# Kernel tuning notes

Measured on AMD Instinct MI355X. Metric: run time of the kernel, lower is better.

The kernel has to match this reference:

```python
import jax, jax.numpy as jnp
import numpy as np

N = 50000      # nodes
E = 800000     # directed edges (avg degree 16)
M = 10000      # hyperedges
P = 200000     # hypergraph incidence pairs (~4 per vertex)
D_IN = 64
D_OUT = 64
NEG_SLOPE = 0.2


def setup_inputs() -> dict:
    key = jax.random.key(0)
    ks = jax.random.split(key, 9)
    X = jax.random.normal(ks[0], (N, D_IN), jnp.float32)
    theta_w = jax.random.normal(ks[1], (D_OUT, D_IN), jnp.float32) / np.float32(np.sqrt(D_IN))
    theta_b = jax.random.normal(ks[2], (D_OUT,), jnp.float32) * 0.01
    a_src = jax.random.normal(ks[3], (D_OUT,), jnp.float32) / np.float32(np.sqrt(D_OUT))
    a_dst = jax.random.normal(ks[4], (D_OUT,), jnp.float32) / np.float32(np.sqrt(D_OUT))
    e_src = jax.random.randint(ks[5], (E,), 0, N, jnp.int32)
    e_dst = jax.random.randint(ks[6], (E,), 0, N, jnp.int32)
    inc_v = jax.random.randint(ks[7], (P,), 0, N, jnp.int32)
    inc_e = jax.random.randint(ks[8], (P,), 0, M, jnp.int32)
    return {"X": X, "theta_w": theta_w, "theta_b": theta_b, "a_src": a_src,
            "a_dst": a_dst, "e_src": e_src, "e_dst": e_dst,
            "inc_v": inc_v, "inc_e": inc_e}


def reference(X, theta_w, theta_b, a_src, a_dst, e_src, e_dst, inc_v, inc_e):
    # theta: Linear(in, out)
    Xp = X @ theta_w.T + theta_b                      # [N, D_OUT]
    # atten_src/atten_dst: Linear(out, 1, bias=False) -> per-node scalars
    s_src = Xp @ a_src                                # [N]
    s_dst = Xp @ a_dst                                # [N]
    # edge attention scores: gather + leaky_relu (dropout = identity in eval)
    score = jax.nn.leaky_relu(s_src[e_src] + s_dst[e_dst], NEG_SLOPE)  # [E]
    # segment softmax over incoming edges of each destination node
    seg_max = jax.ops.segment_max(score, e_dst, num_segments=N)
    seg_max = jax.lax.stop_gradient(jnp.where(jnp.isfinite(seg_max), seg_max, 0.0))
    w = jnp.exp(score - seg_max[e_dst])               # [E]
    denom = jax.ops.segment_sum(w, e_dst, num_segments=N)
    w = w / denom[e_dst]
    # weighted scatter-sum of source features (g.v2v softmax_then_sum)
    X_g = jax.ops.segment_sum(w[:, None] * Xp[e_src], e_dst, num_segments=N)
    # HGNN smoothing: D_v^{-1/2} H D_e^{-1} H^T D_v^{-1/2} Xp  (unit hyperedge weights)
    ones_p = jnp.ones((P,), Xp.dtype)
    dv = jax.ops.segment_sum(ones_p, inc_v, num_segments=N)
    de = jax.ops.segment_sum(ones_p, inc_e, num_segments=M)
    dv_isqrt = jnp.where(dv > 0, jax.lax.rsqrt(jnp.maximum(dv, 1.0)), 0.0)
    de_inv = jnp.where(de > 0, 1.0 / jnp.maximum(de, 1.0), 0.0)
    Xs = Xp * dv_isqrt[:, None]                        # [N, D_OUT]
    He = jax.ops.segment_sum(Xs[inc_v], inc_e, num_segments=M) * de_inv[:, None]  # [M, D_OUT]
    X_hg = jax.ops.segment_sum(He[inc_e], inc_v, num_segments=N) * dv_isqrt[:, None]
    X1 = (X_g + X_hg) * 0.5
    return jax.nn.elu(X1)
```

## Files before the change

### kernel.cpp

```cpp
#include <hip/hip_runtime.h>
#include <math.h>

#define DD 64

typedef __attribute__((ext_vector_type(8))) short bf16x8;
typedef __attribute__((ext_vector_type(4))) float f32x4;

__device__ __forceinline__ unsigned short f2bf(float x) {
    unsigned int u = __float_as_uint(x);
    u += 0x7fffu + ((u >> 16) & 1u);
    return (unsigned short)(u >> 16);
}
__device__ __forceinline__ float bflo(unsigned int u) { return __uint_as_float(u << 16); }
__device__ __forceinline__ float bfhi(unsigned int u) { return __uint_as_float(u & 0xffff0000u); }

__global__ __launch_bounds__(256) void k_gemm(
    const float* __restrict__ X, const float* __restrict__ W,
    const float* __restrict__ bias, const float* __restrict__ a_src,
    const float* __restrict__ a_dst, unsigned short* __restrict__ Xp_bf,
    float* __restrict__ s_src, float* __restrict__ s_dst, int N)
{
    int t = threadIdx.x;
    int lane = t & 63;
    int col = lane & 15;
    int kq  = lane >> 4;
    int rowbase = kq * 4;

    bf16x8 bfrag[4][2];
    float bj[4], asr[4], adr[4];
    #pragma unroll
    for (int jt = 0; jt < 4; ++jt) {
        int j = jt * 16 + col;
        #pragma unroll
        for (int ks = 0; ks < 2; ++ks) {
            const float* wp = W + j * DD + ks * 32 + kq * 8;
            float4 w0 = *(const float4*)wp;
            float4 w1 = *(const float4*)(wp + 4);
            bf16x8 bb;
            bb[0] = (short)f2bf(w0.x); bb[1] = (short)f2bf(w0.y);
            bb[2] = (short)f2bf(w0.z); bb[3] = (short)f2bf(w0.w);
            bb[4] = (short)f2bf(w1.x); bb[5] = (short)f2bf(w1.y);
            bb[6] = (short)f2bf(w1.z); bb[7] = (short)f2bf(w1.w);
            bfrag[jt][ks] = bb;
        }
        bj[jt]  = bias[j];
        asr[jt] = a_src[j];
        adr[jt] = a_dst[j];
    }

    int wave  = (blockIdx.x * 256 + t) >> 6;
    int nwave = (gridDim.x * 256) >> 6;
    int ntiles = (N + 15) >> 4;
    for (int tile = wave; tile < ntiles; tile += nwave) {
        int r0 = tile * 16;
        int rl = r0 + col;
        if (rl >= N) rl = N - 1;
        const float* xp = X + (size_t)rl * DD + kq * 8;
        float4 x0 = *(const float4*)xp;
        float4 x1 = *(const float4*)(xp + 4);
        float4 x2 = *(const float4*)(xp + 32);
        float4 x3 = *(const float4*)(xp + 36);
        bf16x8 a0, a1;
        a0[0] = (short)f2bf(x0.x); a0[1] = (short)f2bf(x0.y);
        a0[2] = (short)f2bf(x0.z); a0[3] = (short)f2bf(x0.w);
        a0[4] = (short)f2bf(x1.x); a0[5] = (short)f2bf(x1.y);
        a0[6] = (short)f2bf(x1.z); a0[7] = (short)f2bf(x1.w);
        a1[0] = (short)f2bf(x2.x); a1[1] = (short)f2bf(x2.y);
        a1[2] = (short)f2bf(x2.z); a1[3] = (short)f2bf(x2.w);
        a1[4] = (short)f2bf(x3.x); a1[5] = (short)f2bf(x3.y);
        a1[6] = (short)f2bf(x3.z); a1[7] = (short)f2bf(x3.w);

        f32x4 acc[4];
        #pragma unroll
        for (int jt = 0; jt < 4; ++jt) {
            f32x4 c = {bj[jt], bj[jt], bj[jt], bj[jt]};
            c = __builtin_amdgcn_mfma_f32_16x16x32_bf16(a0, bfrag[jt][0], c, 0, 0, 0);
            c = __builtin_amdgcn_mfma_f32_16x16x32_bf16(a1, bfrag[jt][1], c, 0, 0, 0);
            acc[jt] = c;
        }

        int orow = r0 + rowbase;
        #pragma unroll
        for (int jt = 0; jt < 4; ++jt) {
            #pragma unroll
            for (int r = 0; r < 4; ++r) {
                int rr = orow + r;
                if (rr < N)
                    Xp_bf[(size_t)rr * DD + jt * 16 + col] = f2bf(acc[jt][r]);
            }
        }

        float vs[4], vd[4];
        #pragma unroll
        for (int r = 0; r < 4; ++r) {
            vs[r] = acc[0][r] * asr[0] + acc[1][r] * asr[1]
                  + acc[2][r] * asr[2] + acc[3][r] * asr[3];
            vd[r] = acc[0][r] * adr[0] + acc[1][r] * adr[1]
                  + acc[2][r] * adr[2] + acc[3][r] * adr[3];
        }
        #pragma unroll
        for (int off = 1; off < 16; off <<= 1) {
            #pragma unroll
            for (int r = 0; r < 4; ++r) {
                vs[r] += __shfl_xor(vs[r], off, 64);
                vd[r] += __shfl_xor(vd[r], off, 64);
            }
        }
        if (col == 0) {
            #pragma unroll
            for (int r = 0; r < 4; ++r) {
                int rr = orow + r;
                if (rr < N) { s_src[rr] = vs[r]; s_dst[rr] = vd[r]; }
            }
        }
    }
}

__global__ __launch_bounds__(256) void k_count(
    const int* __restrict__ e_dst, const int* __restrict__ inc_e,
    const int* __restrict__ inc_v, int* __restrict__ hist_g,
    int* __restrict__ hist_ie, int* __restrict__ hist_iv,
    int E, int P, int N, int M)
{
    __shared__ int cnt[128];
    int b = blockIdx.x;
    const int* key; int n, B, SH, nblk, blk; int* hist;
    if (b < 256)      { key = e_dst; n = E; B = (N + 511) >> 9; SH = 9; nblk = 256; blk = b;       hist = hist_g;  }
    else if (b < 384) { key = inc_e; n = P; B = (M + 255) >> 8; SH = 8; nblk = 128; blk = b - 256; hist = hist_ie; }
    else              { key = inc_v; n = P; B = (N + 511) >> 9; SH = 9; nblk = 128; blk = b - 384; hist = hist_iv; }
    for (int i = threadIdx.x; i < B; i += 256) cnt[i] = 0;
    __syncthreads();
    int chunk = (n + nblk - 1) / nblk;
    int s = blk * chunk, e = min(n, s + chunk);
    for (int i = s + threadIdx.x; i < e; i += 256)
        atomicAdd(&cnt[key[i] >> SH], 1);
    __syncthreads();
    for (int i = threadIdx.x; i < B; i += 256)
        hist[i * nblk + blk] = cnt[i];
}

__device__ void block_scan4(int* a, int len)
{
    __shared__ int wtot[16];
    __shared__ int carry_s;
    int tid = threadIdx.x, lane = tid & 63, wid = tid >> 6;
    if (tid == 0) carry_s = 0;
    __syncthreads();
    for (int base = 0; base < len; base += 4096) {
        int i0 = base + tid * 4;
        int v[4];
        #pragma unroll
        for (int k = 0; k < 4; ++k) { int i = i0 + k; v[k] = (i < len) ? a[i] : 0; }
        int s = v[0] + v[1] + v[2] + v[3];
        int incl = s;
        #pragma unroll
        for (int off = 1; off < 64; off <<= 1) {
            int t = __shfl_up(incl, off, 64);
            if (lane >= off) incl += t;
        }
        if (lane == 63) wtot[wid] = incl;
        __syncthreads();
        int carry = carry_s;
        int woff = 0;
        for (int wj = 0; wj < wid; ++wj) woff += wtot[wj];
        int excl = carry + woff + incl - s;
        int run = excl;
        #pragma unroll
        for (int k = 0; k < 4; ++k) { int i = i0 + k; if (i < len) a[i] = run; run += v[k]; }
        __syncthreads();
        if (tid == 1023) carry_s = run;
        __syncthreads();
    }
    if (tid == 0) a[len] = carry_s;
}

__global__ __launch_bounds__(1024) void k_scan3(
    int* h0, int l0, int* h1, int l1, int* h2, int l2)
{
    if (blockIdx.x == 0)      block_scan4(h0, l0);
    else if (blockIdx.x == 1) block_scan4(h1, l1);
    else                      block_scan4(h2, l2);
}

__global__ __launch_bounds__(256) void k_scat(
    const int* __restrict__ e_dst, const int* __restrict__ e_src,
    const int* __restrict__ inc_e, const int* __restrict__ inc_v,
    const int* __restrict__ hist_g, const int* __restrict__ hist_ie,
    const int* __restrict__ hist_iv,
    int2* __restrict__ pg, int2* __restrict__ pie, int2* __restrict__ piv,
    int E, int P, int N, int M)
{
    __shared__ int cur[128];
    int b = blockIdx.x;
    const int *key, *pay, *base; int2* out;
    int n, B, SH, nblk, blk;
    if (b < 256)      { key = e_dst; pay = e_src; n = E; B = (N + 511) >> 9; SH = 9; nblk = 256; blk = b;       base = hist_g;  out = pg;  }
    else if (b < 384) { key = inc_e; pay = inc_v; n = P; B = (M + 255) >> 8; SH = 8; nblk = 128; blk = b - 256; base = hist_ie; out = pie; }
    else              { key = inc_v; pay = inc_e; n = P; B = (N + 511) >> 9; SH = 9; nblk = 128; blk = b - 384; base = hist_iv; out = piv; }
    for (int i = threadIdx.x; i < B; i += 256) cur[i] = base[i * nblk + blk];
    __syncthreads();
    int chunk = (n + nblk - 1) / nblk;
    int s = blk * chunk, e = min(n, s + chunk);
    for (int i = s + threadIdx.x; i < e; i += 256) {
        int k = key[i];
        int pos = atomicAdd(&cur[k >> SH], 1);
        out[pos] = make_int2(k, pay[i]);
    }
}

__global__ __launch_bounds__(256) void k_fine(
    const int* __restrict__ hist_g, const int* __restrict__ hist_ie,
    const int* __restrict__ hist_iv,
    const int2* __restrict__ pg, const int2* __restrict__ pie,
    const int2* __restrict__ piv,
    int* __restrict__ src_sorted, int* __restrict__ v_sorted,
    int* __restrict__ e_sorted,
    int* __restrict__ start_g, int* __restrict__ start_e,
    int* __restrict__ start_v,
    float* __restrict__ dein, float* __restrict__ dvis, int N, int M)
{
    __shared__ int lh[513];
    __shared__ int lc[512];
    __shared__ int lwt[4];
    __shared__ int lout[10240];
    int Bg = (N + 511) >> 9, Bie = (M + 255) >> 8;
    int b = blockIdx.x, tid = threadIdx.x;
    const int* base; const int2* pr; int* outp; int* startp; float* inv;
    int K, nblk, b0, NK, mode;
    if (b < Bg)            { base = hist_g;  pr = pg;  outp = src_sorted; startp = start_g; inv = nullptr; K = 512; nblk = 256; b0 = b;            NK = N; mode = 0; }
    else if (b < Bg + Bie) { base = hist_ie; pr = pie; outp = v_sorted;   startp = start_e; inv = dein;    K = 256; nblk = 128; b0 = b - Bg;       NK = M; mode = 2; }
    else                   { base = hist_iv; pr = piv; outp = e_sorted;   startp = start_v; inv = dvis;    K = 512; nblk = 128; b0 = b - Bg - Bie; NK = N; mode = 1; }

    int pbase = base[b0 * nblk], pend = base[(b0 + 1) * nblk];
    int cnt = pend - pbase;
    for (int i = tid; i < K; i += 256) { lh[i] = 0; lc[i] = 0; }
    __syncthreads();
    for (int i = tid; i < cnt; i += 256)
        atomicAdd(&lh[pr[pbase + i].x & (K - 1)], 1);
    __syncthreads();

    int per = K >> 8;
    int i0 = tid * per;
    int a0 = lh[i0], a1 = (per == 2) ? lh[i0 + 1] : 0;
    int ssum = a0 + a1;
    int lane = tid & 63, wid = tid >> 6;
    int incl = ssum;
    #pragma unroll
    for (int off = 1; off < 64; off <<= 1) {
        int t = __shfl_up(incl, off, 64);
        if (lane >= off) incl += t;
    }
    if (lane == 63) lwt[wid] = incl;
    __syncthreads();
    int woff = 0;
    for (int wj = 0; wj < wid; ++wj) woff += lwt[wj];
    int excl = woff + incl - ssum;
    lh[i0] = excl;
    if (per == 2) lh[i0 + 1] = excl + a0;
    if (tid == 255) lh[K] = excl + ssum;
    __syncthreads();

    for (int i = tid; i < cnt; i += 256) {
        int2 q = pr[pbase + i];
        int kl = q.x & (K - 1);
        int pos = lh[kl] + atomicAdd(&lc[kl], 1);
        lout[pos < 10240 ? pos : 10239] = q.y;
    }
    __syncthreads();
    for (int i = tid; i < cnt; i += 256)
        outp[pbase + i] = lout[i];
    for (int k = tid; k < K; k += 256) {
        int node = b0 * K + k;
        if (node < NK) {
            startp[node] = pbase + lh[k];
            if (mode) {
                int d = lh[k + 1] - lh[k];
                inv[node] = d > 0 ? (mode == 1 ? rsqrtf((float)d) : 1.0f / (float)d) : 0.0f;
            }
        }
    }
    int Bj = (NK + K - 1) / K;
    if (tid == 0 && b0 == Bj - 1) startp[NK] = pend;
}

__global__ __launch_bounds__(256, 8) void k_he(
    const int* __restrict__ start_e, const int* __restrict__ v_sorted,
    const unsigned short* __restrict__ Xp_bf, const float* __restrict__ dvis,
    const float* __restrict__ dein, unsigned short* __restrict__ He_bf, int M)
{
    int lane = threadIdx.x & 63, grp = lane >> 3, gl = lane & 7;
    int e = (blockIdx.x * 256 + threadIdx.x) >> 6;
    if (e >= M) return;
    int s = start_e[e], t = start_e[e + 1];
    float a[8] = {0.f, 0.f, 0.f, 0.f, 0.f, 0.f, 0.f, 0.f};
    for (int i = s + grp; i < t; i += 8) {
        int v = v_sorted[i];
        float dvv = dvis[v];
        uint4 r = *(const uint4*)(Xp_bf + (size_t)v * DD + gl * 8);
        a[0] = fmaf(dvv, bflo(r.x), a[0]); a[1] = fmaf(dvv, bfhi(r.x), a[1]);
        a[2] = fmaf(dvv, bflo(r.y), a[2]); a[3] = fmaf(dvv, bfhi(r.y), a[3]);
        a[4] = fmaf(dvv, bflo(r.z), a[4]); a[5] = fmaf(dvv, bfhi(r.z), a[5]);
        a[6] = fmaf(dvv, bflo(r.w), a[6]); a[7] = fmaf(dvv, bfhi(r.w), a[7]);
    }
    #pragma unroll
    for (int off = 8; off < 64; off <<= 1) {
        #pragma unroll
        for (int j = 0; j < 8; ++j) a[j] += __shfl_xor(a[j], off, 64);
    }
    if (grp == 0) {
        float din = dein[e];
        uint4 o;
        o.x = (unsigned)f2bf(a[0] * din) | ((unsigned)f2bf(a[1] * din) << 16);
        o.y = (unsigned)f2bf(a[2] * din) | ((unsigned)f2bf(a[3] * din) << 16);
        o.z = (unsigned)f2bf(a[4] * din) | ((unsigned)f2bf(a[5] * din) << 16);
        o.w = (unsigned)f2bf(a[6] * din) | ((unsigned)f2bf(a[7] * din) << 16);
        *(uint4*)(He_bf + (size_t)e * DD + gl * 8) = o;
    }
}

__global__ __launch_bounds__(256, 8) void k_out(
    const int* __restrict__ start_g, const int* __restrict__ src_sorted,
    const int* __restrict__ start_v, const int* __restrict__ e_sorted,
    const float* __restrict__ ssrc, const float* __restrict__ sdst,
    const unsigned short* __restrict__ Xp_bf, const unsigned short* __restrict__ He_bf,
    const float* __restrict__ dvis, float* __restrict__ out, int N)
{
    int lane = threadIdx.x & 63, grp = lane >> 3, gl = lane & 7;
    int n = (blockIdx.x * 256 + threadIdx.x) >> 6;
    if (n >= N) return;

    float sd = sdst[n];
    int gs = start_g[n], ge = start_g[n + 1];
    float g[8] = {0.f, 0.f, 0.f, 0.f, 0.f, 0.f, 0.f, 0.f};
    float wsum = 0.f;
    for (int i = gs + grp; i < ge; i += 8) {
        int s = src_sorted[i];
        float sc = ssrc[s] + sd;
        sc = sc > 0.f ? sc : 0.2f * sc;
        float w = __expf(sc);
        wsum += w;
        uint4 r = *(const uint4*)(Xp_bf + (size_t)s * DD + gl * 8);
        g[0] = fmaf(w, bflo(r.x), g[0]); g[1] = fmaf(w, bfhi(r.x), g[1]);
        g[2] = fmaf(w, bflo(r.y), g[2]); g[3] = fmaf(w, bfhi(r.y), g[3]);
        g[4] = fmaf(w, bflo(r.z), g[4]); g[5] = fmaf(w, bfhi(r.z), g[5]);
        g[6] = fmaf(w, bflo(r.w), g[6]); g[7] = fmaf(w, bfhi(r.w), g[7]);
    }
    int vs = start_v[n], ve = start_v[n + 1];
    float h[8] = {0.f, 0.f, 0.f, 0.f, 0.f, 0.f, 0.f, 0.f};
    for (int i = vs + grp; i < ve; i += 8) {
        int e = e_sorted[i];
        uint4 r = *(const uint4*)(He_bf + (size_t)e * DD + gl * 8);
        h[0] += bflo(r.x); h[1] += bfhi(r.x);
        h[2] += bflo(r.y); h[3] += bfhi(r.y);
        h[4] += bflo(r.z); h[5] += bfhi(r.z);
        h[6] += bflo(r.w); h[7] += bfhi(r.w);
    }
    #pragma unroll
    for (int off = 8; off < 64; off <<= 1) {
        #pragma unroll
        for (int j = 0; j < 8; ++j) {
            g[j] += __shfl_xor(g[j], off, 64);
            h[j] += __shfl_xor(h[j], off, 64);
        }
        wsum += __shfl_xor(wsum, off, 64);
    }
    if (grp == 0) {
        float winv = (ge > gs) ? 1.0f / wsum : 0.f;
        float dvn = dvis[n];
        float o[8];
        #pragma unroll
        for (int j = 0; j < 8; ++j) {
            float x = 0.5f * (g[j] * winv + dvn * h[j]);
            o[j] = x > 0.f ? x : expm1f(x);
        }
        float* op = out + (size_t)n * DD + gl * 8;
        *(float4*)op       = make_float4(o[0], o[1], o[2], o[3]);
        *(float4*)(op + 4) = make_float4(o[4], o[5], o[6], o[7]);
    }
}

extern "C" void kernel_launch(void* const* d_in, const int* in_sizes, int n_in,
                              void* d_out, int out_size, void* d_ws, size_t ws_size,
                              hipStream_t stream)
{
    const float* X     = (const float*)d_in[0];
    const float* W     = (const float*)d_in[1];
    const float* bias  = (const float*)d_in[2];
    const float* a_src = (const float*)d_in[3];
    const float* a_dst = (const float*)d_in[4];
    const int* e_src   = (const int*)d_in[5];
    const int* e_dst   = (const int*)d_in[6];
    const int* inc_v   = (const int*)d_in[7];
    const int* inc_e   = (const int*)d_in[8];
    float* out = (float*)d_out;

    const int N = in_sizes[0] / DD;
    const int E = in_sizes[5];
    const int P = in_sizes[7];
    const int M = 10000;
    const int Bg = (N + 511) >> 9, Bie = (M + 255) >> 8, Biv = Bg;

    char* p = (char*)d_ws;
    unsigned short* Xp_bf = (unsigned short*)p; p += (size_t)N * DD * 2;
    unsigned short* He_bf = (unsigned short*)p; p += (size_t)M * DD * 2;
    int2* pg  = (int2*)p; p += (size_t)E * 8;
    int2* pie = (int2*)p; p += (size_t)P * 8;
    int2* piv = (int2*)p; p += (size_t)P * 8;
    int* src_sorted = (int*)p; p += (size_t)E * 4;
    int* v_sorted   = (int*)p; p += (size_t)P * 4;
    int* e_sorted   = (int*)p; p += (size_t)P * 4;
    float* ssrc = (float*)p; p += (size_t)N * 4;
    float* sdst = (float*)p; p += (size_t)N * 4;
    float* dvis = (float*)p; p += (size_t)N * 4;
    float* dein = (float*)p; p += (size_t)M * 4;
    int* start_g = (int*)p; p += (size_t)(N + 1) * 4;
    int* start_v = (int*)p; p += (size_t)(N + 1) * 4;
    int* start_e = (int*)p; p += (size_t)(M + 1) * 4;
    int* hist_g  = (int*)p; p += (size_t)(Bg * 256 + 1) * 4;
    int* hist_ie = (int*)p; p += (size_t)(Bie * 128 + 1) * 4;
    int* hist_iv = (int*)p; p += (size_t)(Biv * 128 + 1) * 4;

    k_gemm<<<196, 256, 0, stream>>>(X, W, bias, a_src, a_dst, Xp_bf, ssrc, sdst, N);
    k_count<<<512, 256, 0, stream>>>(e_dst, inc_e, inc_v, hist_g, hist_ie, hist_iv,
                                     E, P, N, M);
    k_scan3<<<3, 1024, 0, stream>>>(hist_g, Bg * 256, hist_ie, Bie * 128,
                                    hist_iv, Biv * 128);
    k_scat<<<512, 256, 0, stream>>>(e_dst, e_src, inc_e, inc_v,
                                    hist_g, hist_ie, hist_iv, pg, pie, piv,
                                    E, P, N, M);
    k_fine<<<Bg + Bie + Biv, 256, 0, stream>>>(hist_g, hist_ie, hist_iv, pg, pie, piv,
                                               src_sorted, v_sorted, e_sorted,
                                               start_g, start_e, start_v,
                                               dein, dvis, N, M);
    k_he<<<(M * DD + 255) / 256, 256, 0, stream>>>(start_e, v_sorted, Xp_bf, dvis,
                                                   dein, He_bf, M);
    k_out<<<(N * DD + 255) / 256, 256, 0, stream>>>(start_g, src_sorted, start_v,
                                                    e_sorted, ssrc, sdst, Xp_bf,
                                                    He_bf, dvis, out, N);
}
```

Baseline: 117.3 us.

## Fuse GEMM with histogram count, pack sort pairs to 32-bit, unroll gathers

Merges the independent histogram-count kernel into the GEMM launch as extra blocks, which removes one launch and lets the two run concurrently. Packs each key/payload pair into a single 32-bit word (low key bits plus payload shifted), halving the traffic of the bucket scatter and fine-sort passes. Unrolls the gather loops in the hyperedge and output kernels by two so more loads are in flight. Packing assumes payload indices fit in 32 minus the shift bits, which holds for these sizes.

```diff
diff --git a/kernel.cpp b/kernel.cpp
--- a/kernel.cpp
+++ b/kernel.cpp
@@ -14,12 +14,36 @@
 __device__ __forceinline__ float bflo(unsigned int u) { return __uint_as_float(u << 16); }
 __device__ __forceinline__ float bfhi(unsigned int u) { return __uint_as_float(u & 0xffff0000u); }
 
-__global__ __launch_bounds__(256) void k_gemm(
+#define GEMM_BLOCKS 196
+
+__global__ __launch_bounds__(256) void k_gemm_count(
     const float* __restrict__ X, const float* __restrict__ W,
     const float* __restrict__ bias, const float* __restrict__ a_src,
     const float* __restrict__ a_dst, unsigned short* __restrict__ Xp_bf,
-    float* __restrict__ s_src, float* __restrict__ s_dst, int N)
-{
+    float* __restrict__ s_src, float* __restrict__ s_dst,
+    const int* __restrict__ e_dst, const int* __restrict__ inc_e,
+    const int* __restrict__ inc_v, int* __restrict__ hist_g,
+    int* __restrict__ hist_ie, int* __restrict__ hist_iv,
+    int N, int E, int P, int M)
+{
+    if (blockIdx.x >= GEMM_BLOCKS) {
+        __shared__ int cnt[128];
+        int b = blockIdx.x - GEMM_BLOCKS;
+        const int* key; int n, B, SH, nblk, blk; int* hist;
+        if (b < 256)      { key = e_dst; n = E; B = (N + 511) >> 9; SH = 9; nblk = 256; blk = b;       hist = hist_g;  }
+        else if (b < 384) { key = inc_e; n = P; B = (M + 255) >> 8; SH = 8; nblk = 128; blk = b - 256; hist = hist_ie; }
+        else              { key = inc_v; n = P; B = (N + 511) >> 9; SH = 9; nblk = 128; blk = b - 384; hist = hist_iv; }
+        for (int i = threadIdx.x; i < B; i += 256) cnt[i] = 0;
+        __syncthreads();
+        int chunk = (n + nblk - 1) / nblk;
+        int s = blk * chunk, e = min(n, s + chunk);
+        for (int i = s + threadIdx.x; i < e; i += 256)
+            atomicAdd(&cnt[key[i] >> SH], 1);
+        __syncthreads();
+        for (int i = threadIdx.x; i < B; i += 256)
+            hist[i * nblk + blk] = cnt[i];
+        return;
+    }
     int t = threadIdx.x;
     int lane = t & 63;
     int col = lane & 15;
@@ -49,7 +73,7 @@
     }
 
     int wave  = (blockIdx.x * 256 + t) >> 6;
-    int nwave = (gridDim.x * 256) >> 6;
+    int nwave = (GEMM_BLOCKS * 256) >> 6;
     int ntiles = (N + 15) >> 4;
     for (int tile = wave; tile < ntiles; tile += nwave) {
         int r0 = tile * 16;
@@ -116,29 +140,6 @@
     }
 }
 
-__global__ __launch_bounds__(256) void k_count(
-    const int* __restrict__ e_dst, const int* __restrict__ inc_e,
-    const int* __restrict__ inc_v, int* __restrict__ hist_g,
-    int* __restrict__ hist_ie, int* __restrict__ hist_iv,
-    int E, int P, int N, int M)
-{
-    __shared__ int cnt[128];
-    int b = blockIdx.x;
-    const int* key; int n, B, SH, nblk, blk; int* hist;
-    if (b < 256)      { key = e_dst; n = E; B = (N + 511) >> 9; SH = 9; nblk = 256; blk = b;       hist = hist_g;  }
-    else if (b < 384) { key = inc_e; n = P; B = (M + 255) >> 8; SH = 8; nblk = 128; blk = b - 256; hist = hist_ie; }
-    else              { key = inc_v; n = P; B = (N + 511) >> 9; SH = 9; nblk = 128; blk = b - 384; hist = hist_iv; }
-    for (int i = threadIdx.x; i < B; i += 256) cnt[i] = 0;
-    __syncthreads();
-    int chunk = (n + nblk - 1) / nblk;
-    int s = blk * chunk, e = min(n, s + chunk);
-    for (int i = s + threadIdx.x; i < e; i += 256)
-        atomicAdd(&cnt[key[i] >> SH], 1);
-    __syncthreads();
-    for (int i = threadIdx.x; i < B; i += 256)
-        hist[i * nblk + blk] = cnt[i];
-}
-
 __device__ void block_scan4(int* a, int len)
 {
     __shared__ int wtot[16];
@@ -187,12 +188,13 @@
     const int* __restrict__ inc_e, const int* __restrict__ inc_v,
     const int* __restrict__ hist_g, const int* __restrict__ hist_ie,
     const int* __restrict__ hist_iv,
-    int2* __restrict__ pg, int2* __restrict__ pie, int2* __restrict__ piv,
+    unsigned int* __restrict__ pg, unsigned int* __restrict__ pie,
+    unsigned int* __restrict__ piv,
     int E, int P, int N, int M)
 {
     __shared__ int cur[128];
     int b = blockIdx.x;
-    const int *key, *pay, *base; int2* out;
+    const int *key, *pay, *base; unsigned int* out;
     int n, B, SH, nblk, blk;
     if (b < 256)      { key = e_dst; pay = e_src; n = E; B = (N + 511) >> 9; SH = 9; nblk = 256; blk = b;       base = hist_g;  out = pg;  }
     else if (b < 384) { key = inc_e; pay = inc_v; n = P; B = (M + 255) >> 8; SH = 8; nblk = 128; blk = b - 256; base = hist_ie; out = pie; }
@@ -201,18 +203,19 @@
     __syncthreads();
     int chunk = (n + nblk - 1) / nblk;
     int s = blk * chunk, e = min(n, s + chunk);
+    int mask = (1 << SH) - 1;
     for (int i = s + threadIdx.x; i < e; i += 256) {
         int k = key[i];
         int pos = atomicAdd(&cur[k >> SH], 1);
-        out[pos] = make_int2(k, pay[i]);
+        out[pos] = (unsigned int)(k & mask) | ((unsigned int)pay[i] << SH);
     }
 }
 
 __global__ __launch_bounds__(256) void k_fine(
     const int* __restrict__ hist_g, const int* __restrict__ hist_ie,
     const int* __restrict__ hist_iv,
-    const int2* __restrict__ pg, const int2* __restrict__ pie,
-    const int2* __restrict__ piv,
+    const unsigned int* __restrict__ pg, const unsigned int* __restrict__ pie,
+    const unsigned int* __restrict__ piv,
     int* __restrict__ src_sorted, int* __restrict__ v_sorted,
     int* __restrict__ e_sorted,
     int* __restrict__ start_g, int* __restrict__ start_e,
@@ -225,18 +228,19 @@
     __shared__ int lout[10240];
     int Bg = (N + 511) >> 9, Bie = (M + 255) >> 8;
     int b = blockIdx.x, tid = threadIdx.x;
-    const int* base; const int2* pr; int* outp; int* startp; float* inv;
+    const int* base; const unsigned int* pr; int* outp; int* startp; float* inv;
     int K, nblk, b0, NK, mode;
     if (b < Bg)            { base = hist_g;  pr = pg;  outp = src_sorted; startp = start_g; inv = nullptr; K = 512; nblk = 256; b0 = b;            NK = N; mode = 0; }
     else if (b < Bg + Bie) { base = hist_ie; pr = pie; outp = v_sorted;   startp = start_e; inv = dein;    K = 256; nblk = 128; b0 = b - Bg;       NK = M; mode = 2; }
     else                   { base = hist_iv; pr = piv; outp = e_sorted;   startp = start_v; inv = dvis;    K = 512; nblk = 128; b0 = b - Bg - Bie; NK = N; mode = 1; }
+    int SHF = (K == 512) ? 9 : 8;
 
     int pbase = base[b0 * nblk], pend = base[(b0 + 1) * nblk];
     int cnt = pend - pbase;
     for (int i = tid; i < K; i += 256) { lh[i] = 0; lc[i] = 0; }
     __syncthreads();
     for (int i = tid; i < cnt; i += 256)
-        atomicAdd(&lh[pr[pbase + i].x & (K - 1)], 1);
+        atomicAdd(&lh[pr[pbase + i] & (K - 1)], 1);
     __syncthreads();
 
     int per = K >> 8;
@@ -261,10 +265,10 @@
     __syncthreads();
 
     for (int i = tid; i < cnt; i += 256) {
-        int2 q = pr[pbase + i];
-        int kl = q.x & (K - 1);
+        unsigned int q = pr[pbase + i];
+        int kl = q & (K - 1);
         int pos = lh[kl] + atomicAdd(&lc[kl], 1);
-        lout[pos < 10240 ? pos : 10239] = q.y;
+        lout[pos < 10240 ? pos : 10239] = (int)(q >> SHF);
     }
     __syncthreads();
     for (int i = tid; i < cnt; i += 256)
@@ -293,14 +297,29 @@
     if (e >= M) return;
     int s = start_e[e], t = start_e[e + 1];
     float a[8] = {0.f, 0.f, 0.f, 0.f, 0.f, 0.f, 0.f, 0.f};
-    for (int i = s + grp; i < t; i += 8) {
-        int v = v_sorted[i];
-        float dvv = dvis[v];
-        uint4 r = *(const uint4*)(Xp_bf + (size_t)v * DD + gl * 8);
-        a[0] = fmaf(dvv, bflo(r.x), a[0]); a[1] = fmaf(dvv, bfhi(r.x), a[1]);
-        a[2] = fmaf(dvv, bflo(r.y), a[2]); a[3] = fmaf(dvv, bfhi(r.y), a[3]);
-        a[4] = fmaf(dvv, bflo(r.z), a[4]); a[5] = fmaf(dvv, bfhi(r.z), a[5]);
-        a[6] = fmaf(dvv, bflo(r.w), a[6]); a[7] = fmaf(dvv, bfhi(r.w), a[7]);
+    int i = s + grp;
+    for (; i + 8 < t; i += 16) {
+        int v0 = v_sorted[i], v1 = v_sorted[i + 8];
+        uint4 r0 = *(const uint4*)(Xp_bf + (size_t)v0 * DD + gl * 8);
+        uint4 r1 = *(const uint4*)(Xp_bf + (size_t)v1 * DD + gl * 8);
+        float d0 = dvis[v0], d1 = dvis[v1];
+        a[0] = fmaf(d0, bflo(r0.x), a[0]); a[1] = fmaf(d0, bfhi(r0.x), a[1]);
+        a[2] = fmaf(d0, bflo(r0.y), a[2]); a[3] = fmaf(d0, bfhi(r0.y), a[3]);
+        a[4] = fmaf(d0, bflo(r0.z), a[4]); a[5] = fmaf(d0, bfhi(r0.z), a[5]);
+        a[6] = fmaf(d0, bflo(r0.w), a[6]); a[7] = fmaf(d0, bfhi(r0.w), a[7]);
+        a[0] = fmaf(d1, bflo(r1.x), a[0]); a[1] = fmaf(d1, bfhi(r1.x), a[1]);
+        a[2] = fmaf(d1, bflo(r1.y), a[2]); a[3] = fmaf(d1, bfhi(r1.y), a[3]);
+        a[4] = fmaf(d1, bflo(r1.z), a[4]); a[5] = fmaf(d1, bfhi(r1.z), a[5]);
+        a[6] = fmaf(d1, bflo(r1.w), a[6]); a[7] = fmaf(d1, bfhi(r1.w), a[7]);
+    }
+    if (i < t) {
+        int v0 = v_sorted[i];
+        uint4 r0 = *(const uint4*)(Xp_bf + (size_t)v0 * DD + gl * 8);
+        float d0 = dvis[v0];
+        a[0] = fmaf(d0, bflo(r0.x), a[0]); a[1] = fmaf(d0, bfhi(r0.x), a[1]);
+        a[2] = fmaf(d0, bflo(r0.y), a[2]); a[3] = fmaf(d0, bfhi(r0.y), a[3]);
+        a[4] = fmaf(d0, bflo(r0.z), a[4]); a[5] = fmaf(d0, bfhi(r0.z), a[5]);
+        a[6] = fmaf(d0, bflo(r0.w), a[6]); a[7] = fmaf(d0, bfhi(r0.w), a[7]);
     }
     #pragma unroll
     for (int off = 8; off < 64; off <<= 1) {
@@ -333,27 +352,54 @@
     int gs = start_g[n], ge = start_g[n + 1];
     float g[8] = {0.f, 0.f, 0.f, 0.f, 0.f, 0.f, 0.f, 0.f};
     float wsum = 0.f;
-    for (int i = gs + grp; i < ge; i += 8) {
-        int s = src_sorted[i];
-        float sc = ssrc[s] + sd;
-        sc = sc > 0.f ? sc : 0.2f * sc;
-        float w = __expf(sc);
-        wsum += w;
-        uint4 r = *(const uint4*)(Xp_bf + (size_t)s * DD + gl * 8);
-        g[0] = fmaf(w, bflo(r.x), g[0]); g[1] = fmaf(w, bfhi(r.x), g[1]);
-        g[2] = fmaf(w, bflo(r.y), g[2]); g[3] = fmaf(w, bfhi(r.y), g[3]);
-        g[4] = fmaf(w, bflo(r.z), g[4]); g[5] = fmaf(w, bfhi(r.z), g[5]);
-        g[6] = fmaf(w, bflo(r.w), g[6]); g[7] = fmaf(w, bfhi(r.w), g[7]);
+    int i = gs + grp;
+    for (; i + 8 < ge; i += 16) {
+        int s0 = src_sorted[i], s1 = src_sorted[i + 8];
+        uint4 r0 = *(const uint4*)(Xp_bf + (size_t)s0 * DD + gl * 8);
+        uint4 r1 = *(const uint4*)(Xp_bf + (size_t)s1 * DD + gl * 8);
+        float sc0 = ssrc[s0] + sd; sc0 = sc0 > 0.f ? sc0 : 0.2f * sc0;
+        float sc1 = ssrc[s1] + sd; sc1 = sc1 > 0.f ? sc1 : 0.2f * sc1;
+        float w0 = __expf(sc0), w1 = __expf(sc1);
+        wsum += w0 + w1;
+        g[0] = fmaf(w0, bflo(r0.x), g[0]); g[1] = fmaf(w0, bfhi(r0.x), g[1]);
+        g[2] = fmaf(w0, bflo(r0.y), g[2]); g[3] = fmaf(w0, bfhi(r0.y), g[3]);
+        g[4] = fmaf(w0, bflo(r0.z), g[4]); g[5] = fmaf(w0, bfhi(r0.z), g[5]);
+        g[6] = fmaf(w0, bflo(r0.w), g[6]); g[7] = fmaf(w0, bfhi(r0.w), g[7]);
+        g[0] = fmaf(w1, bflo(r1.x), g[0]); g[1] = fmaf(w1, bfhi(r1.x), g[1]);
+        g[2] = fmaf(w1, bflo(r1.y), g[2]); g[3] = fmaf(w1, bfhi(r1.y), g[3]);
+        g[4] = fmaf(w1, bflo(r1.z), g[4]); g[5] = fmaf(w1, bfhi(r1.z), g[5]);
+        g[6] = fmaf(w1, bflo(r1.w), g[6]); g[7] = fmaf(w1, bfhi(r1.w), g[7]);
+    }
+    if (i < ge) {
+        int s0 = src_sorted[i];
+        uint4 r0 = *(const uint4*)(Xp_bf + (size_t)s0 * DD + gl * 8);
+        float sc0 = ssrc[s0] + sd; sc0 = sc0 > 0.f ? sc0 : 0.2f * sc0;
+        float w0 = __expf(sc0);
+        wsum += w0;
+        g[0] = fmaf(w0, bflo(r0.x), g[0]); g[1] = fmaf(w0, bfhi(r0.x), g[1]);
+        g[2] = fmaf(w0, bflo(r0.y), g[2]); g[3] = fmaf(w0, bfhi(r0.y), g[3]);
+        g[4] = fmaf(w0, bflo(r0.z), g[4]); g[5] = fmaf(w0, bfhi(r0.z), g[5]);
+        g[6] = fmaf(w0, bflo(r0.w), g[6]); g[7] = fmaf(w0, bfhi(r0.w), g[7]);
     }
     int vs = start_v[n], ve = start_v[n + 1];
     float h[8] = {0.f, 0.f, 0.f, 0.f, 0.f, 0.f, 0.f, 0.f};
-    for (int i = vs + grp; i < ve; i += 8) {
-        int e = e_sorted[i];
-        uint4 r = *(const uint4*)(He_bf + (size_t)e * DD + gl * 8);
-        h[0] += bflo(r.x); h[1] += bfhi(r.x);
-        h[2] += bflo(r.y); h[3] += bfhi(r.y);
-        h[4] += bflo(r.z); h[5] += bfhi(r.z);
-        h[6] += bflo(r.w); h[7] += bfhi(r.w);
+    i = vs + grp;
+    for (; i + 8 < ve; i += 16) {
+        int e0 = e_sorted[i], e1 = e_sorted[i + 8];
+        uint4 r0 = *(const uint4*)(He_bf + (size_t)e0 * DD + gl * 8);
+        uint4 r1 = *(const uint4*)(He_bf + (size_t)e1 * DD + gl * 8);
+        h[0] += bflo(r0.x) + bflo(r1.x); h[1] += bfhi(r0.x) + bfhi(r1.x);
+        h[2] += bflo(r0.y) + bflo(r1.y); h[3] += bfhi(r0.y) + bfhi(r1.y);
+        h[4] += bflo(r0.z) + bflo(r1.z); h[5] += bfhi(r0.z) + bfhi(r1.z);
+        h[6] += bflo(r0.w) + bflo(r1.w); h[7] += bfhi(r0.w) + bfhi(r1.w);
+    }
+    if (i < ve) {
+        int e0 = e_sorted[i];
+        uint4 r0 = *(const uint4*)(He_bf + (size_t)e0 * DD + gl * 8);
+        h[0] += bflo(r0.x); h[1] += bfhi(r0.x);
+        h[2] += bflo(r0.y); h[3] += bfhi(r0.y);
+        h[4] += bflo(r0.z); h[5] += bfhi(r0.z);
+        h[6] += bflo(r0.w); h[7] += bfhi(r0.w);
     }
     #pragma unroll
     for (int off = 8; off < 64; off <<= 1) {
@@ -403,9 +449,9 @@
     char* p = (char*)d_ws;
     unsigned short* Xp_bf = (unsigned short*)p; p += (size_t)N * DD * 2;
     unsigned short* He_bf = (unsigned short*)p; p += (size_t)M * DD * 2;
-    int2* pg  = (int2*)p; p += (size_t)E * 8;
-    int2* pie = (int2*)p; p += (size_t)P * 8;
-    int2* piv = (int2*)p; p += (size_t)P * 8;
+    unsigned int* pg  = (unsigned int*)p; p += (size_t)E * 4;
+    unsigned int* pie = (unsigned int*)p; p += (size_t)P * 4;
+    unsigned int* piv = (unsigned int*)p; p += (size_t)P * 4;
     int* src_sorted = (int*)p; p += (size_t)E * 4;
     int* v_sorted   = (int*)p; p += (size_t)P * 4;
     int* e_sorted   = (int*)p; p += (size_t)P * 4;
@@ -420,9 +466,9 @@
     int* hist_ie = (int*)p; p += (size_t)(Bie * 128 + 1) * 4;
     int* hist_iv = (int*)p; p += (size_t)(Biv * 128 + 1) * 4;
 
-    k_gemm<<<196, 256, 0, stream>>>(X, W, bias, a_src, a_dst, Xp_bf, ssrc, sdst, N);
-    k_count<<<512, 256, 0, stream>>>(e_dst, inc_e, inc_v, hist_g, hist_ie, hist_iv,
-                                     E, P, N, M);
+    k_gemm_count<<<GEMM_BLOCKS + 512, 256, 0, stream>>>(
+        X, W, bias, a_src, a_dst, Xp_bf, ssrc, sdst,
+        e_dst, inc_e, inc_v, hist_g, hist_ie, hist_iv, N, E, P, M);
     k_scan3<<<3, 1024, 0, stream>>>(hist_g, Bg * 256, hist_ie, Bie * 128,
                                     hist_iv, Biv * 128);
     k_scat<<<512, 256, 0, stream>>>(e_dst, e_src, inc_e, inc_v,
```

After: 108.5 us. 7.5% less time.
